# Performance work log

Measured on AMD Instinct MI355X. Metric: run time of the kernel, lower is better.

Reference implementation:

```python
import jax, jax.numpy as jnp
import numpy as np

D_LATENT = 8
N_CENTERS = 48
CHANNELS = 64
PM_STEPS = 4
DT, BETA, CLAMP = 0.12, 1.0, 3.0
SIGMA_E, SIGMA_I, K_E, K_I, GAIN = 0.6, 1.2, 0.8, 1.0, 0.06


def setup_inputs() -> dict:
    key = jax.random.key(0)
    ks = jax.random.split(key, 12)
    B = 8192
    x = jax.random.normal(ks[0], (B, 784), dtype=jnp.float32)
    # encoder params (torch Linear default-ish init scale)
    W1 = jax.random.normal(ks[1], (784, 256), dtype=jnp.float32) * (1.0 / np.sqrt(784))
    b1 = jnp.zeros((256,), jnp.float32)
    W2 = jax.random.normal(ks[2], (256, D_LATENT), dtype=jnp.float32) * (1.0 / np.sqrt(256))
    b2 = jnp.zeros((D_LATENT,), jnp.float32)
    centers = jax.random.normal(ks[3], (N_CENTERS, D_LATENT), dtype=jnp.float32) * 0.7
    mus = jnp.ones((N_CENTERS,), jnp.float32) * 0.4
    projW = jax.random.normal(ks[4], (D_LATENT, CHANNELS), dtype=jnp.float32) * (1.0 / np.sqrt(D_LATENT))
    projb = jnp.zeros((CHANNELS,), jnp.float32)
    roW = jax.random.normal(ks[5], (CHANNELS, 10), dtype=jnp.float32) * (1.0 / np.sqrt(CHANNELS))
    rob = jnp.zeros((10,), jnp.float32)
    return {"x": x, "W1": W1, "b1": b1, "W2": W2, "b2": b2,
            "centers": centers, "mus": mus, "projW": projW, "projb": projb,
            "roW": roW, "rob": rob, "T": 5}


def _pm_field(z, centers, mus):
    # one PMField forward: `PM_STEPS` gradient-flow steps on z [B, d]
    for _ in range(PM_STEPS):
        diff = z[:, None, :] - centers[None, :, :]            # [B, C, d]
        r2 = jnp.sum(diff * diff, axis=-1) + 1e-4              # [B, C]
        r = jnp.sqrt(r2)
        n = 1.0 + jnp.sum(mus[None, :] / r, axis=1)            # [B]
        g = -jnp.sum(mus[None, :, None] * diff / (r * r2)[:, :, None], axis=1)  # [B, d]
        z = z + DT * BETA * (g / n[:, None])
        z = jnp.clip(z, -CLAMP, CLAMP)
    return z


def _lateral_ei(z, h):
    # kernel computed with no_grad in torch -> stop_gradient here
    sq = jnp.sum(z * z, axis=1)                                # [B]
    dist2 = jnp.maximum(sq[:, None] + sq[None, :] - 2.0 * (z @ z.T), 0.0)
    Ke = K_E * jnp.exp(-dist2 / (2.0 * SIGMA_E ** 2))
    Ki = K_I * jnp.exp(-dist2 / (2.0 * SIGMA_I ** 2))
    K = Ke - Ki
    K = K / (jnp.sum(K, axis=1, keepdims=True) + 1e-6)
    K = jax.lax.stop_gradient(K)
    return GAIN * (K @ h)


def reference(x, W1, b1, W2, b2, centers, mus, projW, projb, roW, rob, T):
    z = jnp.tanh(x @ W1 + b1) @ W2 + b2                        # encoder -> [B, d]
    h = jnp.zeros((x.shape[0], CHANNELS), x.dtype)
    logits = None
    for _ in range(T):
        z = _pm_field(z, centers, mus)
        h = 0.9 * h + 0.1 * jnp.tanh(z @ projW + projb)
        h = h + _lateral_ei(z, h)
        logits = h @ roW + rob
    return logits, z, h
```

## Files before the change

kernel.cpp:

```cpp
#include <hip/hip_runtime.h>
#include <hip/hip_bf16.h>
#include <math.h>

#define B_N      8192
#define IN_DIM   784
#define HID      256
#define DL       8
#define NC       48
#define CH       64
#define NCLS     10
#define T_ITERS  5
#define TILES    128

#define DT_      0.12f
#define CLAMP_   3.0f
#define GAIN_    0.06f
#define SQIL2    0.70776814f
#define ONE_BF16 0x3F80u

#if defined(__has_builtin)
#if __has_builtin(__builtin_amdgcn_exp2f)
#define EXP2(x) __builtin_amdgcn_exp2f(x)
#endif
#endif
#ifndef EXP2
#define EXP2(x) exp2f(x)
#endif

typedef __attribute__((ext_vector_type(8))) short short8v;
typedef __attribute__((ext_vector_type(4))) float f32x4;

__device__ __forceinline__ unsigned int pack_bf16_rhu(float lo, float hi) {
    unsigned int b0 = __builtin_bit_cast(unsigned int, lo);
    unsigned int b1 = __builtin_bit_cast(unsigned int, hi);
    return ((b0 + 0x8000u) >> 16) | ((b1 + 0x8000u) & 0xFFFF0000u);
}
__device__ __forceinline__ unsigned short bf16_1(float x) {
    return (unsigned short)((__builtin_bit_cast(unsigned int, x) + 0x8000u) >> 16);
}
__device__ __forceinline__ float bf16_to_f(unsigned short h) {
    return __builtin_bit_cast(float, ((unsigned int)h) << 16);
}

__device__ __forceinline__ void z_split(const float4 a, const float4 b,
                                        uint4& Whi, uint4& Wlo, unsigned int& Wc)
{
    float u[8] = {SQIL2*a.x, SQIL2*a.y, SQIL2*a.z, SQIL2*a.w,
                  SQIL2*b.x, SQIL2*b.y, SQIL2*b.z, SQIL2*b.w};
    float sq = 0.f;
    #pragma unroll
    for (int d = 0; d < 8; ++d) sq = fmaf(u[d], u[d], sq);
    float cn = -0.5f * sq;
    unsigned short hi[8]; float lo[8];
    #pragma unroll
    for (int d = 0; d < 8; ++d) {
        hi[d] = bf16_1(u[d]);
        lo[d] = u[d] - bf16_to_f(hi[d]);
    }
    unsigned short ch_ = bf16_1(cn);
    unsigned short cl_ = bf16_1(cn - bf16_to_f(ch_));
    Whi.x = (unsigned int)hi[0] | ((unsigned int)hi[1] << 16);
    Whi.y = (unsigned int)hi[2] | ((unsigned int)hi[3] << 16);
    Whi.z = (unsigned int)hi[4] | ((unsigned int)hi[5] << 16);
    Whi.w = (unsigned int)hi[6] | ((unsigned int)hi[7] << 16);
    Wlo.x = pack_bf16_rhu(lo[0], lo[1]); Wlo.y = pack_bf16_rhu(lo[2], lo[3]);
    Wlo.z = pack_bf16_rhu(lo[4], lo[5]); Wlo.w = pack_bf16_rhu(lo[6], lo[7]);
    Wc = (unsigned int)ch_ | ((unsigned int)cl_ << 16);
}

__global__ __launch_bounds__(256) void k_gemm1_tanh(
    const float* __restrict__ x, const float* __restrict__ W1,
    const float* __restrict__ b1, float* __restrict__ H1)
{
    __shared__ float As[2][16][68];
    __shared__ float Bs[2][16][64];
    const int tid = threadIdx.x;
    const int row0 = blockIdx.x * 64;
    const int col0 = blockIdx.y * 64;
    const int tr = tid >> 4, tc = tid & 15;
    const int am = tid >> 2, akq = tid & 3;
    const int bkk = tid >> 4, bn4 = tid & 15;
    float acc[4][4] = {};

    {
        float4 va = *(const float4*)(x + (size_t)(row0 + am) * IN_DIM + akq * 4);
        float4 vb = *(const float4*)(W1 + (size_t)bkk * HID + col0 + bn4 * 4);
        As[0][akq*4+0][am] = va.x; As[0][akq*4+1][am] = va.y;
        As[0][akq*4+2][am] = va.z; As[0][akq*4+3][am] = va.w;
        *(float4*)(&Bs[0][bkk][bn4*4]) = vb;
    }

    const int NK = IN_DIM / 16;
    #pragma unroll 1
    for (int ks = 0; ks < NK; ++ks) {
        const int cur = ks & 1;
        const bool more = (ks + 1 < NK);
        float4 va, vb;
        if (more) {
            const int k0 = (ks + 1) * 16;
            va = *(const float4*)(x + (size_t)(row0 + am) * IN_DIM + k0 + akq * 4);
            vb = *(const float4*)(W1 + (size_t)(k0 + bkk) * HID + col0 + bn4 * 4);
        }
        __syncthreads();
        #pragma unroll
        for (int kk = 0; kk < 16; ++kk) {
            float4 a = *(const float4*)(&As[cur][kk][tr*4]);
            float4 b = *(const float4*)(&Bs[cur][kk][tc*4]);
            float av[4] = {a.x, a.y, a.z, a.w};
            float bv[4] = {b.x, b.y, b.z, b.w};
            #pragma unroll
            for (int i = 0; i < 4; ++i)
                #pragma unroll
                for (int j = 0; j < 4; ++j)
                    acc[i][j] += av[i] * bv[j];
        }
        if (more) {
            const int nb = cur ^ 1;
            As[nb][akq*4+0][am] = va.x; As[nb][akq*4+1][am] = va.y;
            As[nb][akq*4+2][am] = va.z; As[nb][akq*4+3][am] = va.w;
            *(float4*)(&Bs[nb][bkk][bn4*4]) = vb;
        }
    }

    const float4 b1c = *(const float4*)(b1 + col0 + tc * 4);
    const float bb[4] = {b1c.x, b1c.y, b1c.z, b1c.w};
    #pragma unroll
    for (int i = 0; i < 4; ++i) {
        int r = row0 + tr*4 + i;
        float4 hv;
        hv.x = tanhf(acc[i][0] + bb[0]);
        hv.y = tanhf(acc[i][1] + bb[1]);
        hv.z = tanhf(acc[i][2] + bb[2]);
        hv.w = tanhf(acc[i][3] + bb[3]);
        *(float4*)(H1 + (size_t)r * HID + col0 + tc * 4) = hv;
    }
}

__global__ __launch_bounds__(256) void k_gemm2(
    const float* __restrict__ H1, const float* __restrict__ W2,
    const float* __restrict__ b2, float* __restrict__ zbuf)
{
    __shared__ float W2s[HID][DL];
    const int tid = threadIdx.x;
    for (int l = tid; l < HID * DL; l += 256) W2s[l >> 3][l & 7] = W2[l];
    __syncthreads();
    const int row = blockIdx.x * 32 + (tid >> 3);
    const int d = tid & 7;
    float acc = b2[d];
    const float* hr = H1 + (size_t)row * HID;
    for (int k = 0; k < HID; k += 4) {
        float4 hv = *(const float4*)(hr + k);
        acc += hv.x * W2s[k][d] + hv.y * W2s[k+1][d]
             + hv.z * W2s[k+2][d] + hv.w * W2s[k+3][d];
    }
    zbuf[(size_t)row * DL + d] = acc;
}

template<int S, bool HP>
__global__ __launch_bounds__(256) void k_pm_proj(
    const float* __restrict__ centers, const float* __restrict__ mus,
    const float* __restrict__ projW, const float* __restrict__ projb,
    float* __restrict__ zbuf, float* __restrict__ hB,
    unsigned short* __restrict__ hTb,
    const float* __restrict__ pAcc, const float* __restrict__ pDen)
{
    __shared__ float4 cs4[NC][2];
    __shared__ float mu_s[NC];
    __shared__ float pW[DL][CH];
    __shared__ float pb[CH];
    const int tid = threadIdx.x;
    for (int l = tid; l < NC * 2; l += 256) cs4[l >> 1][l & 1] = ((const float4*)centers)[l];
    if (tid < NC) mu_s[tid] = mus[tid];
    for (int l = tid; l < DL * CH; l += 256) pW[l >> 6][l & 63] = projW[l];
    if (tid < CH) pb[tid] = projb[tid];
    __syncthreads();

    const int rloc = tid >> 3;
    const int dl = tid & 7;
    const int row = blockIdx.x * 32 + rloc;

    float4 cza[6], czb[6];
    float mur[6];
    #pragma unroll
    for (int k = 0; k < 6; ++k) {
        cza[k] = cs4[dl + 8*k][0];
        czb[k] = cs4[dl + 8*k][1];
        mur[k] = mu_s[dl + 8*k];
    }

    float z[8];
    {
        const float4* zp = (const float4*)(zbuf + (size_t)row * DL);
        float4 a = zp[0], b = zp[1];
        z[0]=a.x; z[1]=a.y; z[2]=a.z; z[3]=a.w;
        z[4]=b.x; z[5]=b.y; z[6]=b.z; z[7]=b.w;
    }

    #pragma unroll
    for (int step = 0; step < 4; ++step) {
        float np = 0.f;
        float gp[8] = {0,0,0,0,0,0,0,0};
        #pragma unroll
        for (int k = 0; k < 6; ++k) {
            float d0 = z[0]-cza[k].x, d1 = z[1]-cza[k].y;
            float d2 = z[2]-cza[k].z, d3 = z[3]-cza[k].w;
            float d4 = z[4]-czb[k].x, d5 = z[5]-czb[k].y;
            float d6 = z[6]-czb[k].z, d7 = z[7]-czb[k].w;
            float r2 = 1e-4f;
            r2 = fmaf(d0,d0,r2); r2 = fmaf(d1,d1,r2);
            r2 = fmaf(d2,d2,r2); r2 = fmaf(d3,d3,r2);
            r2 = fmaf(d4,d4,r2); r2 = fmaf(d5,d5,r2);
            r2 = fmaf(d6,d6,r2); r2 = fmaf(d7,d7,r2);
            float r = sqrtf(r2);
            float mr = mur[k] / r;
            np += mr;
            float t = mr / r2;
            gp[0] = fmaf(-t, d0, gp[0]); gp[1] = fmaf(-t, d1, gp[1]);
            gp[2] = fmaf(-t, d2, gp[2]); gp[3] = fmaf(-t, d3, gp[3]);
            gp[4] = fmaf(-t, d4, gp[4]); gp[5] = fmaf(-t, d5, gp[5]);
            gp[6] = fmaf(-t, d6, gp[6]); gp[7] = fmaf(-t, d7, gp[7]);
        }
        #pragma unroll
        for (int m = 1; m < 8; m <<= 1) {
            np += __shfl_xor(np, m);
            #pragma unroll
            for (int d = 0; d < 8; ++d) gp[d] += __shfl_xor(gp[d], m);
        }
        float s = DT_ / (1.f + np);
        #pragma unroll
        for (int d = 0; d < 8; ++d) {
            z[d] = fmaf(s, gp[d], z[d]);
            z[d] = fminf(fmaxf(z[d], -CLAMP_), CLAMP_);
        }
    }

    {
        float zout = z[0];
        #pragma unroll
        for (int d = 1; d < 8; ++d) zout = (dl == d) ? z[d] : zout;
        zbuf[(size_t)row * DL + dl] = zout;
    }

    const int c0 = dl * 8;
    float hin[8];
    if (HP) {
        float den = 1e-6f;
        #pragma unroll
        for (int s = 0; s < S; ++s) den += pDen[s * B_N + row];
        float inv = GAIN_ / den;
        #pragma unroll
        for (int q = 0; q < 2; ++q) {
            float4 a = {0.f, 0.f, 0.f, 0.f};
            #pragma unroll
            for (int s = 0; s < S; ++s) {
                float4 p = *(const float4*)(pAcc + (size_t)s * B_N * CH
                                            + (size_t)row * CH + c0 + q * 4);
                a.x += p.x; a.y += p.y; a.z += p.z; a.w += p.w;
            }
            float4 hm = *(const float4*)(hB + (size_t)row * CH + c0 + q * 4);
            hin[q*4+0] = fmaf(inv, a.x, hm.x);
            hin[q*4+1] = fmaf(inv, a.y, hm.y);
            hin[q*4+2] = fmaf(inv, a.z, hm.z);
            hin[q*4+3] = fmaf(inv, a.w, hm.w);
        }
    } else {
        #pragma unroll
        for (int k = 0; k < 8; ++k) hin[k] = 0.f;
    }
    #pragma unroll
    for (int k = 0; k < 8; ++k) {
        int c = c0 + k;
        float s = pb[c];
        #pragma unroll
        for (int dd = 0; dd < DL; ++dd) s = fmaf(z[dd], pW[dd][c], s);
        hin[k] = 0.9f * hin[k] + 0.1f * tanhf(s);
    }
    float4 o0 = {hin[0], hin[1], hin[2], hin[3]};
    float4 o1 = {hin[4], hin[5], hin[6], hin[7]};
    *(float4*)(hB + (size_t)row * CH + c0)     = o0;
    *(float4*)(hB + (size_t)row * CH + c0 + 4) = o1;

    {
        const int jl = row & 63;
        const int colp = (jl & 35) | ((jl & 12) << 1) | ((jl & 16) >> 2);
        const size_t tb = (size_t)(row & ~63) + colp;
        #pragma unroll
        for (int k = 0; k < 8; ++k)
            hTb[(size_t)(c0 + k) * B_N + tb] = bf16_1(hin[k]);
    }
}

template<int S>
__global__ __launch_bounds__(128, 2) void k_lateral(
    const float* __restrict__ zbuf, const unsigned short* __restrict__ hTb,
    float* __restrict__ pAcc, float* __restrict__ pDen)
{
    __shared__ __align__(16) unsigned short zA[2][64 * 24];
    __shared__ __align__(16) unsigned short hsT[2][CH][72];
    const int tid  = threadIdx.x;
    const int lane = tid & 63;
    const int wv   = tid >> 6;
    const int l15  = lane & 15;
    const int g    = lane >> 4;
    const int rowbase = blockIdx.x * 64;
    const int t0 = (TILES * blockIdx.y) / S;
    const int t1 = (TILES * (blockIdx.y + 1)) / S;
    const int chS = tid >> 1, hfS = tid & 1;

    short8v bZa, bZb;
    #pragma unroll
    for (int setb = 0; setb < 2; ++setb) {
        const int irow = rowbase + 32 * wv + 16 * setb + l15;
        const float4* zp = (const float4*)(zbuf + (size_t)irow * DL);
        uint4 Whi, Wlo; unsigned int Wc;
        z_split(zp[0], zp[1], Whi, Wlo, Wc);
        union { unsigned int u[4]; short8v v; } uh, ul, ua;
        uh.u[0]=Whi.x; uh.u[1]=Whi.y; uh.u[2]=Whi.z; uh.u[3]=Whi.w;
        ul.u[0]=Wlo.x; ul.u[1]=Wlo.y; ul.u[2]=Wlo.z; ul.u[3]=Wlo.w;
        ua.u[0] = ONE_BF16 | (ONE_BF16 << 16);
        ua.u[1] = Wc; ua.u[2] = 0; ua.u[3] = 0;
        short8v bz = (g == 2) ? ul.v : ((g == 3) ? ua.v : uh.v);
        if (setb == 0) bZa = bz; else bZb = bz;
    }
    const int offsh = (g == 1) ? 8 : ((g == 3) ? 16 : 0);

    short8v bones;
    {
        union { unsigned int u[4]; short8v v; } uo;
        uo.u[0] = uo.u[1] = uo.u[2] = uo.u[3] = ONE_BF16 | (ONE_BF16 << 16);
        bones = uo.v;
    }

    f32x4 accA0 = {0,0,0,0}, accA1 = {0,0,0,0}, accA2 = {0,0,0,0}, accA3 = {0,0,0,0};
    f32x4 accB0 = {0,0,0,0}, accB1 = {0,0,0,0}, accB2 = {0,0,0,0}, accB3 = {0,0,0,0};
    f32x4 acc4A = {0,0,0,0}, acc4B = {0,0,0,0};
    const f32x4 zc = {0,0,0,0};

    {
        const int jb = t0 * 64;
        if (tid < 64) {
            const float4* zp = (const float4*)(zbuf + (size_t)(jb + tid) * DL);
            uint4 Whi, Wlo; unsigned int Wc;
            z_split(zp[0], zp[1], Whi, Wlo, Wc);
            uint4 W2v; W2v.x = Wc; W2v.y = ONE_BF16 | (ONE_BF16 << 16);
            W2v.z = 0; W2v.w = 0;
            unsigned short* dst = &zA[0][tid * 24];
            *(uint4*)(dst)      = Whi;
            *(uint4*)(dst + 8)  = Wlo;
            *(uint4*)(dst + 16) = W2v;
        }
        const unsigned short* hs = hTb + (size_t)chS * B_N + jb + hfS * 32;
        *(uint4*)(&hsT[0][chS][hfS*32])      = *(const uint4*)(hs);
        *(uint4*)(&hsT[0][chS][hfS*32 + 8])  = *(const uint4*)(hs + 8);
        *(uint4*)(&hsT[0][chS][hfS*32 + 16]) = *(const uint4*)(hs + 16);
        *(uint4*)(&hsT[0][chS][hfS*32 + 24]) = *(const uint4*)(hs + 24);
    }

    #pragma unroll 1
    for (int jt = t0; jt < t1; ++jt) {
        const int cur = (jt - t0) & 1;
        const bool more = (jt + 1 < t1);
        uint4 h0n, h1n, h2n, h3n;
        float4 zna, znb;
        if (more) {
            const int jb2 = (jt + 1) * 64;
            const unsigned short* hs = hTb + (size_t)chS * B_N + jb2 + hfS * 32;
            h0n = *(const uint4*)(hs);
            h1n = *(const uint4*)(hs + 8);
            h2n = *(const uint4*)(hs + 16);
            h3n = *(const uint4*)(hs + 24);
            if (tid < 64) {
                const float4* zp = (const float4*)(zbuf + (size_t)(jb2 + tid) * DL);
                zna = zp[0]; znb = zp[1];
            }
        }
        __syncthreads();

        f32x4 gacA[4], gacB[4];
        __builtin_amdgcn_s_setprio(1);
        #pragma unroll
        for (int t = 0; t < 4; ++t) {
            short8v az = *(const short8v*)(&zA[cur][(t * 16 + l15) * 24 + offsh]);
            gacA[t] = __builtin_amdgcn_mfma_f32_16x16x32_bf16(az, bZa, zc, 0, 0, 0);
            gacB[t] = __builtin_amdgcn_mfma_f32_16x16x32_bf16(az, bZb, zc, 0, 0, 0);
        }
        __builtin_amdgcn_s_setprio(0);

        short8v afrA[2], afrB[2];
        #pragma unroll
        for (int kb = 0; kb < 2; ++kb) {
            float w8[8];
            #pragma unroll
            for (int m = 0; m < 8; ++m) {
                float out = gacA[2 * kb + (m >> 2)][m & 3];
                float e1 = EXP2(out);
                float e2 = e1 * e1;
                float e4 = e2 * e2;
                float e8 = e4 * e4;
                w8[m] = fmaf(0.8f, e8, -e2);
            }
            union { unsigned int u[4]; short8v v; } uf;
            uf.u[0] = pack_bf16_rhu(w8[0], w8[1]);
            uf.u[1] = pack_bf16_rhu(w8[2], w8[3]);
            uf.u[2] = pack_bf16_rhu(w8[4], w8[5]);
            uf.u[3] = pack_bf16_rhu(w8[6], w8[7]);
            afrA[kb] = uf.v;
        }
        #pragma unroll
        for (int kb = 0; kb < 2; ++kb) {
            float w8[8];
            #pragma unroll
            for (int m = 0; m < 8; ++m) {
                float out = gacB[2 * kb + (m >> 2)][m & 3];
                float e1 = EXP2(out);
                float e2 = e1 * e1;
                float e4 = e2 * e2;
                float e8 = e4 * e4;
                w8[m] = fmaf(0.8f, e8, -e2);
            }
            union { unsigned int u[4]; short8v v; } uf;
            uf.u[0] = pack_bf16_rhu(w8[0], w8[1]);
            uf.u[1] = pack_bf16_rhu(w8[2], w8[3]);
            uf.u[2] = pack_bf16_rhu(w8[4], w8[5]);
            uf.u[3] = pack_bf16_rhu(w8[6], w8[7]);
            afrB[kb] = uf.v;
        }

        __builtin_amdgcn_s_setprio(1);
        #pragma unroll
        for (int kb = 0; kb < 2; ++kb) {
            const int jo = kb * 32 + g * 8;
            short8v b0 = *(const short8v*)&hsT[cur][ 0 + l15][jo];
            short8v b1 = *(const short8v*)&hsT[cur][16 + l15][jo];
            short8v b2 = *(const short8v*)&hsT[cur][32 + l15][jo];
            short8v b3 = *(const short8v*)&hsT[cur][48 + l15][jo];
            accA0 = __builtin_amdgcn_mfma_f32_16x16x32_bf16(afrA[kb], b0, accA0, 0, 0, 0);
            accA1 = __builtin_amdgcn_mfma_f32_16x16x32_bf16(afrA[kb], b1, accA1, 0, 0, 0);
            accA2 = __builtin_amdgcn_mfma_f32_16x16x32_bf16(afrA[kb], b2, accA2, 0, 0, 0);
            accA3 = __builtin_amdgcn_mfma_f32_16x16x32_bf16(afrA[kb], b3, accA3, 0, 0, 0);
            accB0 = __builtin_amdgcn_mfma_f32_16x16x32_bf16(afrB[kb], b0, accB0, 0, 0, 0);
            accB1 = __builtin_amdgcn_mfma_f32_16x16x32_bf16(afrB[kb], b1, accB1, 0, 0, 0);
            accB2 = __builtin_amdgcn_mfma_f32_16x16x32_bf16(afrB[kb], b2, accB2, 0, 0, 0);
            accB3 = __builtin_amdgcn_mfma_f32_16x16x32_bf16(afrB[kb], b3, accB3, 0, 0, 0);
            acc4A = __builtin_amdgcn_mfma_f32_16x16x32_bf16(afrA[kb], bones, acc4A, 0, 0, 0);
            acc4B = __builtin_amdgcn_mfma_f32_16x16x32_bf16(afrB[kb], bones, acc4B, 0, 0, 0);
        }
        __builtin_amdgcn_s_setprio(0);

        if (more) {
            const int nb = cur ^ 1;
            if (tid < 64) {
                uint4 Whi, Wlo; unsigned int Wc;
                z_split(zna, znb, Whi, Wlo, Wc);
                uint4 W2v; W2v.x = Wc; W2v.y = ONE_BF16 | (ONE_BF16 << 16);
                W2v.z = 0; W2v.w = 0;
                unsigned short* dst = &zA[nb][tid * 24];
                *(uint4*)(dst)      = Whi;
                *(uint4*)(dst + 8)  = Wlo;
                *(uint4*)(dst + 16) = W2v;
            }
            *(uint4*)(&hsT[nb][chS][hfS*32])      = h0n;
            *(uint4*)(&hsT[nb][chS][hfS*32 + 8])  = h1n;
            *(uint4*)(&hsT[nb][chS][hfS*32 + 16]) = h2n;
            *(uint4*)(&hsT[nb][chS][hfS*32 + 24]) = h3n;
        }
    }

    float* pA = pAcc + (size_t)blockIdx.y * (B_N * CH) + (size_t)rowbase * CH;
    #pragma unroll
    for (int r = 0; r < 4; ++r) {
        int giA = 32 * wv + g * 4 + r;
        int giB = giA + 16;
        pA[(size_t)giA * CH +  0 + l15] = accA0[r];
        pA[(size_t)giA * CH + 16 + l15] = accA1[r];
        pA[(size_t)giA * CH + 32 + l15] = accA2[r];
        pA[(size_t)giA * CH + 48 + l15] = accA3[r];
        pA[(size_t)giB * CH +  0 + l15] = accB0[r];
        pA[(size_t)giB * CH + 16 + l15] = accB1[r];
        pA[(size_t)giB * CH + 32 + l15] = accB2[r];
        pA[(size_t)giB * CH + 48 + l15] = accB3[r];
    }
    if (l15 == 0) {
        #pragma unroll
        for (int r = 0; r < 4; ++r) {
            pDen[blockIdx.y * B_N + rowbase + 32 * wv + g * 4 + r]      = acc4A[r];
            pDen[blockIdx.y * B_N + rowbase + 32 * wv + 16 + g * 4 + r] = acc4B[r];
        }
    }
}

template<int S>
__global__ __launch_bounds__(256) void k_logits_h(
    const float* __restrict__ hmid, const float* __restrict__ pAcc,
    const float* __restrict__ pDen, const float* __restrict__ roW,
    const float* __restrict__ rob, float* __restrict__ out_logits,
    float* __restrict__ out_h)
{
    __shared__ float hsh[64][68];
    __shared__ float ro[CH][NCLS];
    __shared__ float rb[NCLS];
    const int tid = threadIdx.x;
    for (int l = tid; l < CH * NCLS; l += 256) ro[l / NCLS][l % NCLS] = roW[l];
    if (tid < NCLS) rb[tid] = rob[tid];
    const int rowbase = blockIdx.x * 64;
    const int r  = tid >> 2;
    const int c0 = (tid & 3) * 16;
    const int row = rowbase + r;
    float den = 1e-6f;
    #pragma unroll
    for (int s = 0; s < S; ++s) den += pDen[s * B_N + row];
    float inv = GAIN_ / den;
    #pragma unroll
    for (int q = 0; q < 4; ++q) {
        float4 a = {0.f, 0.f, 0.f, 0.f};
        #pragma unroll
        for (int s = 0; s < S; ++s) {
            float4 p = *(const float4*)(pAcc + (size_t)s * B_N * CH
                                        + (size_t)row * CH + c0 + q * 4);
            a.x += p.x; a.y += p.y; a.z += p.z; a.w += p.w;
        }
        float4 hm = *(const float4*)(hmid + (size_t)row * CH + c0 + q * 4);
        float4 hv;
        hv.x = fmaf(inv, a.x, hm.x); hv.y = fmaf(inv, a.y, hm.y);
        hv.z = fmaf(inv, a.z, hm.z); hv.w = fmaf(inv, a.w, hm.w);
        *(float4*)(&hsh[r][c0 + q * 4]) = hv;
        *(float4*)(out_h + (size_t)row * CH + c0 + q * 4) = hv;
    }
    __syncthreads();
    for (int idx = tid; idx < 64 * NCLS; idx += 256) {
        int rr = idx / NCLS, o = idx % NCLS;
        float s = rb[o];
        #pragma unroll
        for (int k = 0; k < CH; ++k) s = fmaf(hsh[rr][k], ro[k][o], s);
        out_logits[(size_t)(rowbase + rr) * NCLS + o] = s;
    }
}

template<int S>
static void run_all(const float* x, const float* W1, const float* b1,
                    const float* W2, const float* b2, const float* centers,
                    const float* mus, const float* projW, const float* projb,
                    const float* roW, const float* rob,
                    float* ws, float* out, hipStream_t stream)
{
    float* pAcc = ws;
    float* pDen = ws + (size_t)S * B_N * CH;
    float* zbuf = pDen + (size_t)S * B_N;
    float* hB   = zbuf + B_N * DL;
    unsigned short* hTb = (unsigned short*)(hB + B_N * CH);
    float* H1   = ws;

    float* out_logits = out;
    float* out_z      = out + 81920;
    float* out_h      = out_z + 65536;

    k_gemm1_tanh<<<dim3(B_N / 64, HID / 64), 256, 0, stream>>>(x, W1, b1, H1);
    k_gemm2<<<B_N / 32, 256, 0, stream>>>(H1, W2, b2, zbuf);

    for (int t = 0; t < T_ITERS; ++t) {
        if (t == 0)
            k_pm_proj<S, false><<<B_N / 32, 256, 0, stream>>>(
                centers, mus, projW, projb, zbuf, hB, hTb, pAcc, pDen);
        else
            k_pm_proj<S, true><<<B_N / 32, 256, 0, stream>>>(
                centers, mus, projW, projb, zbuf, hB, hTb, pAcc, pDen);
        k_lateral<S><<<dim3(TILES, S), 128, 0, stream>>>(zbuf, hTb, pAcc, pDen);
    }

    k_logits_h<S><<<TILES, 256, 0, stream>>>(hB, pAcc, pDen, roW, rob,
                                             out_logits, out_h);
    hipMemcpyAsync(out_z, zbuf, (size_t)B_N * DL * sizeof(float),
                   hipMemcpyDeviceToDevice, stream);
}

extern "C" void kernel_launch(void* const* d_in, const int* in_sizes, int n_in,
                              void* d_out, int out_size, void* d_ws, size_t ws_size,
                              hipStream_t stream)
{
    const float* x       = (const float*)d_in[0];
    const float* W1      = (const float*)d_in[1];
    const float* b1      = (const float*)d_in[2];
    const float* W2      = (const float*)d_in[3];
    const float* b2      = (const float*)d_in[4];
    const float* centers = (const float*)d_in[5];
    const float* mus     = (const float*)d_in[6];
    const float* projW   = (const float*)d_in[7];
    const float* projb   = (const float*)d_in[8];
    const float* roW     = (const float*)d_in[9];
    const float* rob     = (const float*)d_in[10];

    float* ws  = (float*)d_ws;
    float* out = (float*)d_out;

    const size_t needS8 = ((size_t)8*B_N*CH + 8*B_N + B_N*DL + B_N*CH + B_N*CH/2) * 4;
    const size_t needS4 = ((size_t)4*B_N*CH + 4*B_N + B_N*DL + B_N*CH + B_N*CH/2) * 4;

    if (ws_size >= needS8)
        run_all<8>(x, W1, b1, W2, b2, centers, mus, projW, projb, roW, rob, ws, out, stream);
    else if (ws_size >= needS4)
        run_all<4>(x, W1, b1, W2, b2, centers, mus, projW, projb, roW, rob, ws, out, stream);
    else
        run_all<2>(x, W1, b1, W2, b2, centers, mus, projW, projb, roW, rob, ws, out, stream);
}
```

Measured before the change: 307.0 us.

## Double per-row thread parallelism in PM and lateral kernels

k_pm_proj now uses 16 threads per row, each handling 3 centers, with a wider shuffle reduction and 4 channels per thread. The grid doubles to B/16 blocks. k_lateral moves from 2 waves each handling 32 rows to 4 waves each handling 16 rows, with 256 threads and a wider cooperative h-tile load. This aims to raise occupancy and latency hiding. In exchange it costs more shuffle steps, more blocks and less register-level reuse of each LDS fragment.

```diff
diff --git a/kernel.cpp b/kernel.cpp
--- a/kernel.cpp
+++ b/kernel.cpp
@@ -175,17 +175,17 @@
     if (tid < CH) pb[tid] = projb[tid];
     __syncthreads();
 
-    const int rloc = tid >> 3;
-    const int dl = tid & 7;
-    const int row = blockIdx.x * 32 + rloc;
-
-    float4 cza[6], czb[6];
-    float mur[6];
-    #pragma unroll
-    for (int k = 0; k < 6; ++k) {
-        cza[k] = cs4[dl + 8*k][0];
-        czb[k] = cs4[dl + 8*k][1];
-        mur[k] = mu_s[dl + 8*k];
+    const int rloc = tid >> 4;
+    const int ln   = tid & 15;
+    const int row  = blockIdx.x * 16 + rloc;
+
+    float4 cza[3], czb[3];
+    float mur[3];
+    #pragma unroll
+    for (int k = 0; k < 3; ++k) {
+        cza[k] = cs4[ln + 16*k][0];
+        czb[k] = cs4[ln + 16*k][1];
+        mur[k] = mu_s[ln + 16*k];
     }
 
     float z[8];
@@ -201,7 +201,7 @@
         float np = 0.f;
         float gp[8] = {0,0,0,0,0,0,0,0};
         #pragma unroll
-        for (int k = 0; k < 6; ++k) {
+        for (int k = 0; k < 3; ++k) {
             float d0 = z[0]-cza[k].x, d1 = z[1]-cza[k].y;
             float d2 = z[2]-cza[k].z, d3 = z[3]-cza[k].w;
             float d4 = z[4]-czb[k].x, d5 = z[5]-czb[k].y;
@@ -221,7 +221,7 @@
             gp[6] = fmaf(-t, d6, gp[6]); gp[7] = fmaf(-t, d7, gp[7]);
         }
         #pragma unroll
-        for (int m = 1; m < 8; m <<= 1) {
+        for (int m = 1; m < 16; m <<= 1) {
             np += __shfl_xor(np, m);
             #pragma unroll
             for (int d = 0; d < 8; ++d) gp[d] += __shfl_xor(gp[d], m);
@@ -234,41 +234,38 @@
         }
     }
 
-    {
+    if (ln < 8) {
         float zout = z[0];
         #pragma unroll
-        for (int d = 1; d < 8; ++d) zout = (dl == d) ? z[d] : zout;
-        zbuf[(size_t)row * DL + dl] = zout;
-    }
-
-    const int c0 = dl * 8;
-    float hin[8];
+        for (int d = 1; d < 8; ++d) zout = (ln == d) ? z[d] : zout;
+        zbuf[(size_t)row * DL + ln] = zout;
+    }
+
+    const int c0 = ln * 4;
+    float hin[4];
     if (HP) {
         float den = 1e-6f;
         #pragma unroll
         for (int s = 0; s < S; ++s) den += pDen[s * B_N + row];
         float inv = GAIN_ / den;
-        #pragma unroll
-        for (int q = 0; q < 2; ++q) {
-            float4 a = {0.f, 0.f, 0.f, 0.f};
-            #pragma unroll
-            for (int s = 0; s < S; ++s) {
-                float4 p = *(const float4*)(pAcc + (size_t)s * B_N * CH
-                                            + (size_t)row * CH + c0 + q * 4);
-                a.x += p.x; a.y += p.y; a.z += p.z; a.w += p.w;
-            }
-            float4 hm = *(const float4*)(hB + (size_t)row * CH + c0 + q * 4);
-            hin[q*4+0] = fmaf(inv, a.x, hm.x);
-            hin[q*4+1] = fmaf(inv, a.y, hm.y);
-            hin[q*4+2] = fmaf(inv, a.z, hm.z);
-            hin[q*4+3] = fmaf(inv, a.w, hm.w);
-        }
+        float4 a = {0.f, 0.f, 0.f, 0.f};
+        #pragma unroll
+        for (int s = 0; s < S; ++s) {
+            float4 p = *(const float4*)(pAcc + (size_t)s * B_N * CH
+                                        + (size_t)row * CH + c0);
+            a.x += p.x; a.y += p.y; a.z += p.z; a.w += p.w;
+        }
+        float4 hm = *(const float4*)(hB + (size_t)row * CH + c0);
+        hin[0] = fmaf(inv, a.x, hm.x);
+        hin[1] = fmaf(inv, a.y, hm.y);
+        hin[2] = fmaf(inv, a.z, hm.z);
+        hin[3] = fmaf(inv, a.w, hm.w);
     } else {
         #pragma unroll
-        for (int k = 0; k < 8; ++k) hin[k] = 0.f;
-    }
-    #pragma unroll
-    for (int k = 0; k < 8; ++k) {
+        for (int k = 0; k < 4; ++k) hin[k] = 0.f;
+    }
+    #pragma unroll
+    for (int k = 0; k < 4; ++k) {
         int c = c0 + k;
         float s = pb[c];
         #pragma unroll
@@ -276,22 +273,20 @@
         hin[k] = 0.9f * hin[k] + 0.1f * tanhf(s);
     }
     float4 o0 = {hin[0], hin[1], hin[2], hin[3]};
-    float4 o1 = {hin[4], hin[5], hin[6], hin[7]};
-    *(float4*)(hB + (size_t)row * CH + c0)     = o0;
-    *(float4*)(hB + (size_t)row * CH + c0 + 4) = o1;
+    *(float4*)(hB + (size_t)row * CH + c0) = o0;
 
     {
         const int jl = row & 63;
         const int colp = (jl & 35) | ((jl & 12) << 1) | ((jl & 16) >> 2);
         const size_t tb = (size_t)(row & ~63) + colp;
         #pragma unroll
-        for (int k = 0; k < 8; ++k)
+        for (int k = 0; k < 4; ++k)
             hTb[(size_t)(c0 + k) * B_N + tb] = bf16_1(hin[k]);
     }
 }
 
 template<int S>
-__global__ __launch_bounds__(128, 2) void k_lateral(
+__global__ __launch_bounds__(256, 4) void k_lateral(
     const float* __restrict__ zbuf, const unsigned short* __restrict__ hTb,
     float* __restrict__ pAcc, float* __restrict__ pDen)
 {
@@ -305,12 +300,11 @@
     const int rowbase = blockIdx.x * 64;
     const int t0 = (TILES * blockIdx.y) / S;
     const int t1 = (TILES * (blockIdx.y + 1)) / S;
-    const int chS = tid >> 1, hfS = tid & 1;
-
-    short8v bZa, bZb;
-    #pragma unroll
-    for (int setb = 0; setb < 2; ++setb) {
-        const int irow = rowbase + 32 * wv + 16 * setb + l15;
+    const int chS = tid >> 2, segS = tid & 3;
+
+    short8v bZ;
+    {
+        const int irow = rowbase + 16 * wv + l15;
         const float4* zp = (const float4*)(zbuf + (size_t)irow * DL);
         uint4 Whi, Wlo; unsigned int Wc;
         z_split(zp[0], zp[1], Whi, Wlo, Wc);
@@ -319,8 +313,7 @@
         ul.u[0]=Wlo.x; ul.u[1]=Wlo.y; ul.u[2]=Wlo.z; ul.u[3]=Wlo.w;
         ua.u[0] = ONE_BF16 | (ONE_BF16 << 16);
         ua.u[1] = Wc; ua.u[2] = 0; ua.u[3] = 0;
-        short8v bz = (g == 2) ? ul.v : ((g == 3) ? ua.v : uh.v);
-        if (setb == 0) bZa = bz; else bZb = bz;
+        bZ = (g == 2) ? ul.v : ((g == 3) ? ua.v : uh.v);
     }
     const int offsh = (g == 1) ? 8 : ((g == 3) ? 16 : 0);
 
@@ -331,9 +324,8 @@
         bones = uo.v;
     }
 
-    f32x4 accA0 = {0,0,0,0}, accA1 = {0,0,0,0}, accA2 = {0,0,0,0}, accA3 = {0,0,0,0};
-    f32x4 accB0 = {0,0,0,0}, accB1 = {0,0,0,0}, accB2 = {0,0,0,0}, accB3 = {0,0,0,0};
-    f32x4 acc4A = {0,0,0,0}, acc4B = {0,0,0,0};
+    f32x4 acc0 = {0,0,0,0}, acc1 = {0,0,0,0}, acc2 = {0,0,0,0}, acc3 = {0,0,0,0};
+    f32x4 acc4 = {0,0,0,0};
     const f32x4 zc = {0,0,0,0};
 
     {
@@ -349,26 +341,22 @@
             *(uint4*)(dst + 8)  = Wlo;
             *(uint4*)(dst + 16) = W2v;
         }
-        const unsigned short* hs = hTb + (size_t)chS * B_N + jb + hfS * 32;
-        *(uint4*)(&hsT[0][chS][hfS*32])      = *(const uint4*)(hs);
-        *(uint4*)(&hsT[0][chS][hfS*32 + 8])  = *(const uint4*)(hs + 8);
-        *(uint4*)(&hsT[0][chS][hfS*32 + 16]) = *(const uint4*)(hs + 16);
-        *(uint4*)(&hsT[0][chS][hfS*32 + 24]) = *(const uint4*)(hs + 24);
+        const unsigned short* hs = hTb + (size_t)chS * B_N + jb + segS * 16;
+        *(uint4*)(&hsT[0][chS][segS * 16])     = *(const uint4*)(hs);
+        *(uint4*)(&hsT[0][chS][segS * 16 + 8]) = *(const uint4*)(hs + 8);
     }
 
     #pragma unroll 1
     for (int jt = t0; jt < t1; ++jt) {
         const int cur = (jt - t0) & 1;
         const bool more = (jt + 1 < t1);
-        uint4 h0n, h1n, h2n, h3n;
+        uint4 h0n, h1n;
         float4 zna, znb;
         if (more) {
             const int jb2 = (jt + 1) * 64;
-            const unsigned short* hs = hTb + (size_t)chS * B_N + jb2 + hfS * 32;
+            const unsigned short* hs = hTb + (size_t)chS * B_N + jb2 + segS * 16;
             h0n = *(const uint4*)(hs);
             h1n = *(const uint4*)(hs + 8);
-            h2n = *(const uint4*)(hs + 16);
-            h3n = *(const uint4*)(hs + 24);
             if (tid < 64) {
                 const float4* zp = (const float4*)(zbuf + (size_t)(jb2 + tid) * DL);
                 zna = zp[0]; znb = zp[1];
@@ -376,23 +364,22 @@
         }
         __syncthreads();
 
-        f32x4 gacA[4], gacB[4];
+        f32x4 gac[4];
         __builtin_amdgcn_s_setprio(1);
         #pragma unroll
         for (int t = 0; t < 4; ++t) {
             short8v az = *(const short8v*)(&zA[cur][(t * 16 + l15) * 24 + offsh]);
-            gacA[t] = __builtin_amdgcn_mfma_f32_16x16x32_bf16(az, bZa, zc, 0, 0, 0);
-            gacB[t] = __builtin_amdgcn_mfma_f32_16x16x32_bf16(az, bZb, zc, 0, 0, 0);
+            gac[t] = __builtin_amdgcn_mfma_f32_16x16x32_bf16(az, bZ, zc, 0, 0, 0);
         }
         __builtin_amdgcn_s_setprio(0);
 
-        short8v afrA[2], afrB[2];
+        short8v afr[2];
         #pragma unroll
         for (int kb = 0; kb < 2; ++kb) {
             float w8[8];
             #pragma unroll
             for (int m = 0; m < 8; ++m) {
-                float out = gacA[2 * kb + (m >> 2)][m & 3];
+                float out = gac[2 * kb + (m >> 2)][m & 3];
                 float e1 = EXP2(out);
                 float e2 = e1 * e1;
                 float e4 = e2 * e2;
@@ -404,26 +391,7 @@
             uf.u[1] = pack_bf16_rhu(w8[2], w8[3]);
             uf.u[2] = pack_bf16_rhu(w8[4], w8[5]);
             uf.u[3] = pack_bf16_rhu(w8[6], w8[7]);
-            afrA[kb] = uf.v;
-        }
-        #pragma unroll
-        for (int kb = 0; kb < 2; ++kb) {
-            float w8[8];
-            #pragma unroll
-            for (int m = 0; m < 8; ++m) {
-                float out = gacB[2 * kb + (m >> 2)][m & 3];
-                float e1 = EXP2(out);
-                float e2 = e1 * e1;
-                float e4 = e2 * e2;
-                float e8 = e4 * e4;
-                w8[m] = fmaf(0.8f, e8, -e2);
-            }
-            union { unsigned int u[4]; short8v v; } uf;
-            uf.u[0] = pack_bf16_rhu(w8[0], w8[1]);
-            uf.u[1] = pack_bf16_rhu(w8[2], w8[3]);
-            uf.u[2] = pack_bf16_rhu(w8[4], w8[5]);
-            uf.u[3] = pack_bf16_rhu(w8[6], w8[7]);
-            afrB[kb] = uf.v;
+            afr[kb] = uf.v;
         }
 
         __builtin_amdgcn_s_setprio(1);
@@ -434,16 +402,11 @@
             short8v b1 = *(const short8v*)&hsT[cur][16 + l15][jo];
             short8v b2 = *(const short8v*)&hsT[cur][32 + l15][jo];
             short8v b3 = *(const short8v*)&hsT[cur][48 + l15][jo];
-            accA0 = __builtin_amdgcn_mfma_f32_16x16x32_bf16(afrA[kb], b0, accA0, 0, 0, 0);
-            accA1 = __builtin_amdgcn_mfma_f32_16x16x32_bf16(afrA[kb], b1, accA1, 0, 0, 0);
-            accA2 = __builtin_amdgcn_mfma_f32_16x16x32_bf16(afrA[kb], b2, accA2, 0, 0, 0);
-            accA3 = __builtin_amdgcn_mfma_f32_16x16x32_bf16(afrA[kb], b3, accA3, 0, 0, 0);
-            accB0 = __builtin_amdgcn_mfma_f32_16x16x32_bf16(afrB[kb], b0, accB0, 0, 0, 0);
-            accB1 = __builtin_amdgcn_mfma_f32_16x16x32_bf16(afrB[kb], b1, accB1, 0, 0, 0);
-            accB2 = __builtin_amdgcn_mfma_f32_16x16x32_bf16(afrB[kb], b2, accB2, 0, 0, 0);
-            accB3 = __builtin_amdgcn_mfma_f32_16x16x32_bf16(afrB[kb], b3, accB3, 0, 0, 0);
-            acc4A = __builtin_amdgcn_mfma_f32_16x16x32_bf16(afrA[kb], bones, acc4A, 0, 0, 0);
-            acc4B = __builtin_amdgcn_mfma_f32_16x16x32_bf16(afrB[kb], bones, acc4B, 0, 0, 0);
+            acc0 = __builtin_amdgcn_mfma_f32_16x16x32_bf16(afr[kb], b0, acc0, 0, 0, 0);
+            acc1 = __builtin_amdgcn_mfma_f32_16x16x32_bf16(afr[kb], b1, acc1, 0, 0, 0);
+            acc2 = __builtin_amdgcn_mfma_f32_16x16x32_bf16(afr[kb], b2, acc2, 0, 0, 0);
+            acc3 = __builtin_amdgcn_mfma_f32_16x16x32_bf16(afr[kb], b3, acc3, 0, 0, 0);
+            acc4 = __builtin_amdgcn_mfma_f32_16x16x32_bf16(afr[kb], bones, acc4, 0, 0, 0);
         }
         __builtin_amdgcn_s_setprio(0);
 
@@ -459,33 +422,24 @@
                 *(uint4*)(dst + 8)  = Wlo;
                 *(uint4*)(dst + 16) = W2v;
             }
-            *(uint4*)(&hsT[nb][chS][hfS*32])      = h0n;
-            *(uint4*)(&hsT[nb][chS][hfS*32 + 8])  = h1n;
-            *(uint4*)(&hsT[nb][chS][hfS*32 + 16]) = h2n;
-            *(uint4*)(&hsT[nb][chS][hfS*32 + 24]) = h3n;
+            *(uint4*)(&hsT[nb][chS][segS * 16])     = h0n;
+            *(uint4*)(&hsT[nb][chS][segS * 16 + 8]) = h1n;
         }
     }
 
     float* pA = pAcc + (size_t)blockIdx.y * (B_N * CH) + (size_t)rowbase * CH;
     #pragma unroll
     for (int r = 0; r < 4; ++r) {
-        int giA = 32 * wv + g * 4 + r;
-        int giB = giA + 16;
-        pA[(size_t)giA * CH +  0 + l15] = accA0[r];
-        pA[(size_t)giA * CH + 16 + l15] = accA1[r];
-        pA[(size_t)giA * CH + 32 + l15] = accA2[r];
-        pA[(size_t)giA * CH + 48 + l15] = accA3[r];
-        pA[(size_t)giB * CH +  0 + l15] = accB0[r];
-        pA[(size_t)giB * CH + 16 + l15] = accB1[r];
-        pA[(size_t)giB * CH + 32 + l15] = accB2[r];
-        pA[(size_t)giB * CH + 48 + l15] = accB3[r];
+        int gi = 16 * wv + g * 4 + r;
+        pA[(size_t)gi * CH +  0 + l15] = acc0[r];
+        pA[(size_t)gi * CH + 16 + l15] = acc1[r];
+        pA[(size_t)gi * CH + 32 + l15] = acc2[r];
+        pA[(size_t)gi * CH + 48 + l15] = acc3[r];
     }
     if (l15 == 0) {
         #pragma unroll
-        for (int r = 0; r < 4; ++r) {
-            pDen[blockIdx.y * B_N + rowbase + 32 * wv + g * 4 + r]      = acc4A[r];
-            pDen[blockIdx.y * B_N + rowbase + 32 * wv + 16 + g * 4 + r] = acc4B[r];
-        }
+        for (int r = 0; r < 4; ++r)
+            pDen[blockIdx.y * B_N + rowbase + 16 * wv + g * 4 + r] = acc4[r];
     }
 }
 
@@ -559,12 +513,12 @@
 
     for (int t = 0; t < T_ITERS; ++t) {
         if (t == 0)
-            k_pm_proj<S, false><<<B_N / 32, 256, 0, stream>>>(
+            k_pm_proj<S, false><<<B_N / 16, 256, 0, stream>>>(
                 centers, mus, projW, projb, zbuf, hB, hTb, pAcc, pDen);
         else
-            k_pm_proj<S, true><<<B_N / 32, 256, 0, stream>>>(
+            k_pm_proj<S, true><<<B_N / 16, 256, 0, stream>>>(
                 centers, mus, projW, projb, zbuf, hB, hTb, pAcc, pDen);
-        k_lateral<S><<<dim3(TILES, S), 128, 0, stream>>>(zbuf, hTb, pAcc, pDen);
+        k_lateral<S><<<dim3(TILES, S), 256, 0, stream>>>(zbuf, hTb, pAcc, pDen);
     }
 
     k_logits_h<S><<<TILES, 256, 0, stream>>>(hB, pAcc, pDen, roW, rob,
```

After: 297.0 us. 1.03x faster.
